# Kernel tuning notes

Measured on AMD Instinct MI355X. Metric: run time of the kernel, lower is better.

## Reference

```python
import jax, jax.numpy as jnp
import numpy as np

N_UE = 16384
N_AP = 128
E = 2097152
D = 32

relu = jax.nn.relu


def setup_inputs():
    key = jax.random.key(0)
    ks = jax.random.split(key, 24)
    def g(i, shape, s=0.1):
        return jax.random.normal(ks[i], shape, dtype=jnp.float32) * s
    inp = {}
    inp["x_ue"] = jax.random.uniform(ks[0], (N_UE, 1), dtype=jnp.float32)
    inp["e_ua"] = g(1, (E, 2), 1.0)
    inp["e_au"] = g(2, (E, 2), 1.0)
    inp["src"] = jax.random.randint(ks[3], (E,), 0, N_UE)
    inp["dst"] = jax.random.randint(ks[4], (E,), 0, N_AP)
    # layer 1 (Ue2Ap): ue feat dim 1, ap feat dim 0, edge dim 2
    inp["Wm1_ua"] = g(5, (1 + 2, D)); inp["bm1_ua"] = jnp.zeros((D,), jnp.float32)
    inp["Wm1_au"] = g(6, (2, D));     inp["bm1_au"] = jnp.zeros((D,), jnp.float32)
    inp["Wu1_ap"] = g(7, (D, D));     inp["bu1_ap"] = jnp.zeros((D,), jnp.float32)
    inp["Wu1_ue"] = g(8, (1 + D, D)); inp["bu1_ue"] = jnp.zeros((D,), jnp.float32)
    inp["We1_ua"] = g(9, (2 * D + 2, 2));  inp["be1_ua"] = jnp.zeros((2,), jnp.float32)
    inp["We1_au"] = g(10, (2 * D + 2, 2)); inp["be1_au"] = jnp.zeros((2,), jnp.float32)
    # layers 2-4 stacked (all 32 -> 32)
    inp["Wm_ua"] = g(11, (3, D + 2, D)); inp["bm_ua"] = jnp.zeros((3, D), jnp.float32)
    inp["Wm_au"] = g(12, (3, D + 2, D)); inp["bm_au"] = jnp.zeros((3, D), jnp.float32)
    inp["Wu_ap"] = g(13, (3, 2 * D, D)); inp["bu_ap"] = jnp.zeros((3, D), jnp.float32)
    inp["Wu_ue"] = g(14, (3, 2 * D, D)); inp["bu_ue"] = jnp.zeros((3, D), jnp.float32)
    inp["We_ua"] = g(15, (3, 2 * D + 2, 2)); inp["be_ua"] = jnp.zeros((3, 2), jnp.float32)
    inp["We_au"] = g(16, (3, 2 * D + 2, 2)); inp["be_au"] = jnp.zeros((3, 2), jnp.float32)
    # power head: mlp([32,16]) + Lin(16,1) + Sigmoid
    inp["Wp1"] = g(17, (D, 16)); inp["bp1"] = jnp.zeros((16,), jnp.float32)
    inp["Wp2"] = g(18, (16, 1)); inp["bp2"] = jnp.zeros((1,), jnp.float32)
    return inp


def _het_conv(x_ue, x_ap, e_ua, e_au, src, dst,
              Wm_ua, bm_ua, Wm_au, bm_au,
              Wu_ap, bu_ap, Wu_ue, bu_ue,
              We_ua, be_ua, We_au, be_au):
    # ue -> ap: gather src ue feats + edge attr, MLP, scatter-add to ap
    f_ua = jnp.concatenate([x_ue[src], e_ua], axis=1)        # [E, d_ue+2]
    m_ua = relu(f_ua @ Wm_ua + bm_ua)                        # [E, D]
    agg_ap = jax.ops.segment_sum(m_ua, dst, num_segments=N_AP)
    # ap -> ue: ap has no features in layer 1 (dim 0)
    f_au = e_au if x_ap is None else jnp.concatenate([x_ap[dst], e_au], axis=1)
    m_au = relu(f_au @ Wm_au + bm_au)                        # [E, D]
    agg_ue = jax.ops.segment_sum(m_au, src, num_segments=N_UE)
    # node updates
    h_ap = agg_ap if x_ap is None else jnp.concatenate([x_ap, agg_ap], axis=1)
    x_ap_new = relu(h_ap @ Wu_ap + bu_ap)                    # [N_AP, D]
    x_ue_new = relu(jnp.concatenate([x_ue, agg_ue], axis=1) @ Wu_ue + bu_ue)  # [N_UE, D]
    # edge updates (keep edge_dim = 2)
    pair = jnp.concatenate([x_ue_new[src], x_ap_new[dst]], axis=1)  # [E, 2D]
    e_ua_new = relu(jnp.concatenate([pair, e_ua], axis=1) @ We_ua + be_ua)
    e_au_new = relu(jnp.concatenate([pair, e_au], axis=1) @ We_au + be_au)
    return x_ue_new, x_ap_new, e_ua_new, e_au_new


def reference(x_ue, e_ua, e_au, src, dst,
              Wm1_ua, bm1_ua, Wm1_au, bm1_au, Wu1_ap, bu1_ap, Wu1_ue, bu1_ue,
              We1_ua, be1_ua, We1_au, be1_au,
              Wm_ua, bm_ua, Wm_au, bm_au, Wu_ap, bu_ap, Wu_ue, bu_ue,
              We_ua, be_ua, We_au, be_au,
              Wp1, bp1, Wp2, bp2):
    x_ue, x_ap, e_ua, e_au = _het_conv(
        x_ue, None, e_ua, e_au, src, dst,
        Wm1_ua, bm1_ua, Wm1_au, bm1_au, Wu1_ap, bu1_ap, Wu1_ue, bu1_ue,
        We1_ua, be1_ua, We1_au, be1_au)
    for l in range(3):  # conv2, conv3, conv4
        x_ue, x_ap, e_ua, e_au = _het_conv(
            x_ue, x_ap, e_ua, e_au, src, dst,
            Wm_ua[l], bm_ua[l], Wm_au[l], bm_au[l],
            Wu_ap[l], bu_ap[l], Wu_ue[l], bu_ue[l],
            We_ua[l], be_ua[l], We_au[l], be_au[l])
    power = jax.nn.sigmoid(relu(x_ue @ Wp1 + bp1) @ Wp2 + bp2)  # [N_UE, 1]
    ue_out = jnp.concatenate([x_ue[:, :1], power], axis=1)      # [N_UE, 2]
    return ue_out, x_ap, e_ua, e_au
```

## Files before the change

### kernel.cpp

```cpp
#include <hip/hip_runtime.h>
#include <math.h>

#define N_UE 16384
#define N_AP 128
#define NE   2097152
#define NSB  256
#define EPSB (NE / NSB)
#define CHS  8
#define CHD  16
#define NEP  (NE + CHS * N_UE)
#define NCHU (NEP / CHS)
#define NEPD (NE + CHD * N_AP)
#define NCHD (NEPD / CHD)
#define NCHD_AL 131328

#define RFL(x) __int_as_float(__builtin_amdgcn_readfirstlane(__float_as_int(x)))

__global__ __launch_bounds__(256) void prefill(
    int* __restrict__ dtS, int* __restrict__ srcD,
    int* __restrict__ cnS, int* __restrict__ cnD)
{
    int i = blockIdx.x * 256 + threadIdx.x;
    dtS[i] = N_AP;
    if (i < NEPD) srcD[i] = N_UE;
    if (i < NCHU) cnS[i] = -1;
    if (i < NCHD_AL) cnD[i] = -1;
}

__global__ __launch_bounds__(256) void init_kernel(
    const float* __restrict__ x_ue, const float* __restrict__ Wm1_ua,
    const float* __restrict__ bm1_ua, const float* __restrict__ bm1_au,
    float* __restrict__ Qua, float* __restrict__ Pau)
{
    int i = blockIdx.x * 256 + threadIdx.x;
    int d = i & 31;
    Qua[i] = fmaf(x_ue[i >> 5], Wm1_ua[d], bm1_ua[d]);
    if (i < N_AP * 32) Pau[i] = bm1_au[d];
    if (i < 32) { Qua[N_UE * 32 + i] = -1e30f; Pau[N_AP * 32 + i] = -1e30f; }
}

__global__ __launch_bounds__(256) void hist_src(
    const int* __restrict__ src, int* __restrict__ histS)
{
    __shared__ int h[N_UE];
    for (int i = threadIdx.x; i < N_UE; i += 256) h[i] = 0;
    __syncthreads();
    const int beg = blockIdx.x * EPSB;
    for (int e = beg + threadIdx.x; e < beg + EPSB; e += 256)
        atomicAdd(&h[src[e]], 1);
    __syncthreads();
    for (int i = threadIdx.x; i < N_UE; i += 256) histS[blockIdx.x * N_UE + i] = h[i];
}

__global__ __launch_bounds__(256) void colscan_kernel(
    const int* __restrict__ histS, int* __restrict__ baseS, int* __restrict__ cnt)
{
    const int u = blockIdx.x * 256 + threadIdx.x;
    int run = 0;
    for (int b = 0; b < NSB; ++b) {
        int t = histS[b * N_UE + u];
        baseS[b * N_UE + u] = run;
        run += t;
    }
    cnt[u] = run;
}

__global__ __launch_bounds__(256) void scan_src(
    const int* __restrict__ cnt, int* __restrict__ CU)
{
    __shared__ int ps[256];
    __shared__ int ps2[257];
    const int t = threadIdx.x;
    const int b0 = t * (N_UE / 256);
    int s = 0;
    for (int i = 0; i < N_UE / 256; ++i) s += (cnt[b0 + i] + CHS - 1) / CHS;
    ps[t] = s;
    __syncthreads();
    if (t == 0) {
        int r = 0;
        for (int i = 0; i < 256; ++i) { ps2[i] = r; r += ps[i]; }
        ps2[256] = r;
    }
    __syncthreads();
    int r = ps2[t];
    for (int i = 0; i < N_UE / 256; ++i) { CU[b0 + i] = r; r += (cnt[b0 + i] + CHS - 1) / CHS; }
    if (t == 255) CU[N_UE] = ps2[256];
}

__global__ __launch_bounds__(256) void scatter_src(
    const int* __restrict__ src, const int* __restrict__ dst,
    const float2* __restrict__ e0au,
    const int* __restrict__ baseS, const int* __restrict__ CU,
    int* __restrict__ dtS, float2* __restrict__ attS, int* __restrict__ invS)
{
    __shared__ int cursor[N_UE];
    const int b = blockIdx.x;
    for (int i = threadIdx.x; i < N_UE; i += 256)
        cursor[i] = CU[i] * CHS + baseS[b * N_UE + i];
    __syncthreads();
    const int beg = b * EPSB;
    for (int e = beg + threadIdx.x; e < beg + EPSB; e += 256) {
        int s = src[e];
        int pos = atomicAdd(&cursor[s], 1);
        dtS[pos] = dst[e];
        attS[pos] = e0au[e];
        invS[e] = pos;
    }
}

__global__ __launch_bounds__(256) void hist_dst(
    const int* __restrict__ dst, int* __restrict__ histD)
{
    __shared__ int h[N_AP];
    if (threadIdx.x < N_AP) h[threadIdx.x] = 0;
    __syncthreads();
    const int beg = blockIdx.x * EPSB;
    for (int e = beg + threadIdx.x; e < beg + EPSB; e += 256)
        atomicAdd(&h[dst[e]], 1);
    __syncthreads();
    if (threadIdx.x < N_AP) histD[blockIdx.x * N_AP + threadIdx.x] = h[threadIdx.x];
}

__global__ __launch_bounds__(128) void scan_dst(
    const int* __restrict__ histD, int* __restrict__ offsD, int* __restrict__ CA)
{
    __shared__ int colTot[N_AP], colStart[N_AP];
    const int a = threadIdx.x;
    int run = 0;
    for (int b = 0; b < NSB; ++b) {
        offsD[b * N_AP + a] = run;
        run += histD[b * N_AP + a];
    }
    colTot[a] = run;
    __syncthreads();
    if (a == 0) {
        int r = 0;
        for (int i = 0; i < N_AP; ++i) {
            CA[i] = r;
            colStart[i] = r * CHD;
            r += (colTot[i] + CHD - 1) / CHD;
        }
        CA[N_AP] = r;
    }
    __syncthreads();
    const int st = colStart[a];
    for (int b = 0; b < NSB; ++b) offsD[b * N_AP + a] += st;
}

__global__ __launch_bounds__(256) void scatter_dst(
    const int* __restrict__ src, const int* __restrict__ dst,
    const float2* __restrict__ e0ua, const int* __restrict__ offsD,
    int* __restrict__ srcD, float2* __restrict__ attD, int* __restrict__ invD)
{
    __shared__ int cursor[N_AP];
    const int b = blockIdx.x;
    if (threadIdx.x < N_AP) cursor[threadIdx.x] = offsD[b * N_AP + threadIdx.x];
    __syncthreads();
    const int beg = b * EPSB;
    for (int e = beg + threadIdx.x; e < beg + EPSB; e += 256) {
        int dt = dst[e];
        int pos = atomicAdd(&cursor[dt], 1);
        srcD[pos] = src[e];
        attD[pos] = e0ua[e];
        invD[e] = pos;
    }
}

__global__ __launch_bounds__(256) void build_map_src(
    const int* __restrict__ CU, int* __restrict__ cnS)
{
    const int u = blockIdx.x * 256 + threadIdx.x;
    const int c0 = CU[u], c1 = CU[u + 1];
    for (int c = c0; c < c1; ++c) cnS[c] = u;
}

__global__ __launch_bounds__(128) void build_map_dst(
    const int* __restrict__ CA, int* __restrict__ cnD)
{
    const int a = threadIdx.x;
    const int c0 = CA[a], c1 = CA[a + 1];
    for (int c = c0; c < c1; ++c) cnD[c] = a;
}

template<bool EUPD>
__global__ __launch_bounds__(256) void pass_src(
    const int* __restrict__ cnS, const int* __restrict__ dtS,
    float2* __restrict__ attS,
    const float2* __restrict__ RueB, const float2* __restrict__ RapB,
    const float* __restrict__ EcB,
    const float* __restrict__ Pau, const float* __restrict__ cw,
    float* __restrict__ partialU)
{
    const int ch = blockIdx.x * 256 + threadIdx.x;
    const int u = cnS[ch];
    if (u < 0) return;
    float w0v[32], w1v[32];
    #pragma unroll
    for (int d = 0; d < 32; ++d) { w0v[d] = RFL(cw[d]); w1v[d] = RFL(cw[32 + d]); }
    float d00 = 0.f, d01 = 0.f, d10 = 0.f, d11 = 0.f, rbx = 0.f, rby = 0.f;
    if constexpr (EUPD) {
        d00 = RFL(EcB[0]); d01 = RFL(EcB[1]); d10 = RFL(EcB[2]); d11 = RFL(EcB[3]);
        float2 r = RueB[u]; rbx = r.x; rby = r.y;
    }
    const float4* __restrict__ Pau4 = (const float4*)Pau;
    const int base = ch * CHS;
    float4 acc[8];
    #pragma unroll
    for (int q = 0; q < 8; ++q) acc[q] = make_float4(0.f, 0.f, 0.f, 0.f);
    #pragma unroll
    for (int j = 0; j < CHS; ++j) {
        int dt = dtS[base + j];
        float2 a = attS[base + j];
        if constexpr (EUPD) {
            float2 rp = RapB[dt];
            float m0 = fmaxf(rbx + rp.x + a.x * d00 + a.y * d10, 0.f);
            float m1 = fmaxf(rby + rp.y + a.x * d01 + a.y * d11, 0.f);
            a = make_float2(m0, m1);
            attS[base + j] = a;
        }
        const float4* pr = Pau4 + dt * 8;
        #pragma unroll
        for (int q = 0; q < 8; ++q) {
            float4 pv = pr[q];
            acc[q].x += fmaxf(fmaf(a.x, w0v[q*4+0], fmaf(a.y, w1v[q*4+0], pv.x)), 0.f);
            acc[q].y += fmaxf(fmaf(a.x, w0v[q*4+1], fmaf(a.y, w1v[q*4+1], pv.y)), 0.f);
            acc[q].z += fmaxf(fmaf(a.x, w0v[q*4+2], fmaf(a.y, w1v[q*4+2], pv.z)), 0.f);
            acc[q].w += fmaxf(fmaf(a.x, w0v[q*4+3], fmaf(a.y, w1v[q*4+3], pv.w)), 0.f);
        }
    }
    float4* pu = (float4*)(partialU + (size_t)ch * 32);
    #pragma unroll
    for (int q = 0; q < 8; ++q) pu[q] = acc[q];
}

template<bool EUPD>
__global__ __launch_bounds__(256) void pass_dst(
    const int* __restrict__ cnD, const int* __restrict__ srcD,
    float2* __restrict__ attD,
    const float2* __restrict__ RueA, const float2* __restrict__ RapA,
    const float* __restrict__ EcA,
    const float* __restrict__ Qua, const float* __restrict__ cu,
    float* __restrict__ partialA)
{
    const int ch = blockIdx.x * 256 + threadIdx.x;
    const int a = cnD[ch];
    if (a < 0) return;
    float u0v[32], u1v[32];
    #pragma unroll
    for (int d = 0; d < 32; ++d) { u0v[d] = RFL(cu[d]); u1v[d] = RFL(cu[32 + d]); }
    float c00 = 0.f, c01 = 0.f, c10 = 0.f, c11 = 0.f, rax = 0.f, ray = 0.f;
    if constexpr (EUPD) {
        c00 = RFL(EcA[0]); c01 = RFL(EcA[1]); c10 = RFL(EcA[2]); c11 = RFL(EcA[3]);
        float2 r = RapA[a]; rax = r.x; ray = r.y;
    }
    const float4* __restrict__ Qua4 = (const float4*)Qua;
    const int base = ch * CHD;
    float4 acc[8];
    #pragma unroll
    for (int q = 0; q < 8; ++q) acc[q] = make_float4(0.f, 0.f, 0.f, 0.f);
    #pragma unroll 4
    for (int j = 0; j < CHD; ++j) {
        int s = srcD[base + j];
        float2 a2 = attD[base + j];
        if constexpr (EUPD) {
            float2 ru = RueA[s];
            float n0 = fmaxf(rax + ru.x + a2.x * c00 + a2.y * c10, 0.f);
            float n1 = fmaxf(ray + ru.y + a2.x * c01 + a2.y * c11, 0.f);
            a2 = make_float2(n0, n1);
            attD[base + j] = a2;
        }
        const float4* qr = Qua4 + s * 8;
        #pragma unroll
        for (int q = 0; q < 8; ++q) {
            float4 qv = qr[q];
            acc[q].x += fmaxf(fmaf(a2.x, u0v[q*4+0], fmaf(a2.y, u1v[q*4+0], qv.x)), 0.f);
            acc[q].y += fmaxf(fmaf(a2.x, u0v[q*4+1], fmaf(a2.y, u1v[q*4+1], qv.y)), 0.f);
            acc[q].z += fmaxf(fmaf(a2.x, u0v[q*4+2], fmaf(a2.y, u1v[q*4+2], qv.z)), 0.f);
            acc[q].w += fmaxf(fmaf(a2.x, u0v[q*4+3], fmaf(a2.y, u1v[q*4+3], qv.w)), 0.f);
        }
    }
    float4* pa = (float4*)(partialA + (size_t)ch * 32);
    #pragma unroll
    for (int q = 0; q < 8; ++q) pa[q] = acc[q];
}

__global__ __launch_bounds__(256) void reduce_ue(
    const int* __restrict__ CU, const float* __restrict__ partialU,
    float* __restrict__ agg_ue)
{
    const int g   = (blockIdx.x * 256 + threadIdx.x) >> 5;
    const int dim = threadIdx.x & 31;
    const int c0 = CU[g], c1 = CU[g + 1];
    float acc = 0.f;
    for (int c = c0; c < c1; ++c) acc += partialU[(size_t)c * 32 + dim];
    agg_ue[g * 32 + dim] = acc;
}

__global__ __launch_bounds__(256) void final_edge(
    const int* __restrict__ src, const int* __restrict__ dst,
    const int* __restrict__ invS, const int* __restrict__ invD,
    const float2* __restrict__ attS, const float2* __restrict__ attD,
    const float2* __restrict__ RueA, const float2* __restrict__ RueB,
    const float2* __restrict__ RapA, const float2* __restrict__ RapB,
    const float* __restrict__ EcA, const float* __restrict__ EcB,
    float2* __restrict__ out_eua, float2* __restrict__ out_eau)
{
    const int e = blockIdx.x * 256 + threadIdx.x;
    const int s = src[e], dt = dst[e];
    float c00 = EcA[0], c01 = EcA[1], c10 = EcA[2], c11 = EcA[3];
    float d00 = EcB[0], d01 = EcB[1], d10 = EcB[2], d11 = EcB[3];
    float2 eua = attD[invD[e]];
    float2 eau = attS[invS[e]];
    float2 rA = RueA[s], pA = RapA[dt];
    float n0 = fmaxf(rA.x + pA.x + eua.x * c00 + eua.y * c10, 0.f);
    float n1 = fmaxf(rA.y + pA.y + eua.x * c01 + eua.y * c11, 0.f);
    float2 rB = RueB[s], pB = RapB[dt];
    float m0 = fmaxf(rB.x + pB.x + eau.x * d00 + eau.y * d10, 0.f);
    float m1 = fmaxf(rB.y + pB.y + eau.x * d01 + eau.y * d11, 0.f);
    out_eua[e] = make_float2(n0, n1);
    out_eau[e] = make_float2(m0, m1);
}

template<bool FIRST, bool LAST>
__global__ __launch_bounds__(256) void node_ue_kernel(
    const float* __restrict__ x_prev, const float* __restrict__ agg_ue,
    const float* __restrict__ Wu, const float* __restrict__ bu,
    const float* __restrict__ Wm_next, const float* __restrict__ bm_next,
    const float* __restrict__ WeUa, const float* __restrict__ WeUb,
    const float* __restrict__ Wp1, const float* __restrict__ bp1,
    const float* __restrict__ Wp2, const float* __restrict__ bp2,
    float* __restrict__ x_new, float* __restrict__ Qua_next,
    float2* __restrict__ RueA, float2* __restrict__ RueB,
    float2* __restrict__ ue_out)
{
    constexpr int KIN = FIRST ? 33 : 64;
    __shared__ float Wu_s[64 * 32];
    __shared__ float Wm_s[32 * 32];
    __shared__ float WeA_s[64], WeB_s[64];
    __shared__ float bu_s[32], bm_s[32];
    __shared__ float Wp1_s[32 * 16], bp1_s[16], Wp2_s[16];

    const int tid = threadIdx.x;
    for (int i = tid; i < KIN * 32; i += 256) Wu_s[i] = Wu[i];
    if (tid < 32) bu_s[tid] = bu[tid];
    if (!LAST) {
        for (int i = tid; i < 1024; i += 256) Wm_s[i] = Wm_next[i];
        if (tid < 32) bm_s[tid] = bm_next[tid];
    }
    if (tid < 64) { WeA_s[tid] = WeUa[tid]; WeB_s[tid] = WeUb[tid]; }
    if (LAST) {
        for (int i = tid; i < 512; i += 256) Wp1_s[i] = Wp1[i];
        if (tid < 16) { bp1_s[tid] = bp1[tid]; Wp2_s[tid] = Wp2[tid]; }
    }
    __syncthreads();

    const int u = blockIdx.x * 256 + tid;
    float in[KIN];
    if (FIRST) {
        in[0] = x_prev[u];
        #pragma unroll
        for (int k = 0; k < 32; ++k) in[1 + k] = agg_ue[u * 32 + k];
    } else {
        #pragma unroll
        for (int k = 0; k < 32; ++k) in[k] = x_prev[u * 32 + k];
        #pragma unroll
        for (int k = 0; k < 32; ++k) in[32 + k] = agg_ue[u * 32 + k];
    }
    float out[32];
    #pragma unroll
    for (int d = 0; d < 32; ++d) {
        float acc = bu_s[d];
        #pragma unroll
        for (int k = 0; k < KIN; ++k) acc = fmaf(in[k], Wu_s[k * 32 + d], acc);
        out[d] = fmaxf(acc, 0.f);
    }
    #pragma unroll
    for (int d = 0; d < 32; ++d) x_new[u * 32 + d] = out[d];
    if (!LAST) {
        #pragma unroll
        for (int d = 0; d < 32; ++d) {
            float acc = bm_s[d];
            #pragma unroll
            for (int k = 0; k < 32; ++k) acc = fmaf(out[k], Wm_s[k * 32 + d], acc);
            Qua_next[u * 32 + d] = acc;
        }
    }
    float r0 = 0.f, r1 = 0.f, s0 = 0.f, s1 = 0.f;
    #pragma unroll
    for (int k = 0; k < 32; ++k) {
        r0 = fmaf(out[k], WeA_s[k * 2],     r0);
        r1 = fmaf(out[k], WeA_s[k * 2 + 1], r1);
        s0 = fmaf(out[k], WeB_s[k * 2],     s0);
        s1 = fmaf(out[k], WeB_s[k * 2 + 1], s1);
    }
    RueA[u] = make_float2(r0, r1);
    RueB[u] = make_float2(s0, s1);
    if (LAST) {
        float z = bp2[0];
        #pragma unroll
        for (int j = 0; j < 16; ++j) {
            float h = bp1_s[j];
            #pragma unroll
            for (int k = 0; k < 32; ++k) h = fmaf(out[k], Wp1_s[k * 16 + j], h);
            z = fmaf(fmaxf(h, 0.f), Wp2_s[j], z);
        }
        float pw = 1.f / (1.f + expf(-z));
        ue_out[u] = make_float2(out[0], pw);
    }
}

template<bool FIRST, bool LAST>
__global__ __launch_bounds__(256) void node_ap_kernel(
    const float* __restrict__ partialA, const int* __restrict__ CA,
    const float* __restrict__ x_prev,
    const float* __restrict__ Wu, const float* __restrict__ bu,
    const float* __restrict__ Wm_next, const float* __restrict__ bm_next,
    const float* __restrict__ WeA, const float* __restrict__ beA,
    const float* __restrict__ WeB, const float* __restrict__ beB,
    float* __restrict__ x_new, float* __restrict__ Pau_next,
    float2* __restrict__ RapA, float2* __restrict__ RapB)
{
    __shared__ float red[256];
    __shared__ float agg_s[32];
    __shared__ float xnew_s[32];
    const int a = blockIdx.x, tid = threadIdx.x;
    const int d = tid & 31, p0 = tid >> 5;
    const int c0 = CA[a], c1 = CA[a + 1];
    float acc = 0.f;
    for (int p = c0 + p0; p < c1; p += 8)
        acc += partialA[(size_t)p * 32 + d];
    red[tid] = acc;
    __syncthreads();
    if (tid < 32) {
        float s = 0.f;
        #pragma unroll
        for (int i = 0; i < 8; ++i) s += red[i * 32 + tid];
        agg_s[tid] = s;
    }
    __syncthreads();
    if (tid < 32) {
        float acc2 = bu[d];
        if (FIRST) {
            #pragma unroll
            for (int k = 0; k < 32; ++k) acc2 = fmaf(agg_s[k], Wu[k * 32 + d], acc2);
        } else {
            #pragma unroll
            for (int k = 0; k < 32; ++k) acc2 = fmaf(x_prev[a * 32 + k], Wu[k * 32 + d], acc2);
            #pragma unroll
            for (int k = 0; k < 32; ++k) acc2 = fmaf(agg_s[k], Wu[(32 + k) * 32 + d], acc2);
        }
        float xn = fmaxf(acc2, 0.f);
        xnew_s[d] = xn;
        x_new[a * 32 + d] = xn;
    }
    __syncthreads();
    if (!LAST) {
        if (tid < 32) {
            float acc3 = bm_next[d];
            #pragma unroll
            for (int k = 0; k < 32; ++k) acc3 = fmaf(xnew_s[k], Wm_next[k * 32 + d], acc3);
            Pau_next[a * 32 + d] = acc3;
        }
    }
    if (tid == 0) {
        float q0 = beA[0], q1 = beA[1], t0 = beB[0], t1 = beB[1];
        #pragma unroll
        for (int k = 0; k < 32; ++k) {
            q0 = fmaf(xnew_s[k], WeA[k * 2],     q0);
            q1 = fmaf(xnew_s[k], WeA[k * 2 + 1], q1);
            t0 = fmaf(xnew_s[k], WeB[k * 2],     t0);
            t1 = fmaf(xnew_s[k], WeB[k * 2 + 1], t1);
        }
        RapA[a] = make_float2(q0, q1);
        RapB[a] = make_float2(t0, t1);
    }
}

extern "C" void kernel_launch(void* const* d_in, const int* in_sizes, int n_in,
                              void* d_out_v, int out_size, void* d_ws, size_t ws_size,
                              hipStream_t stream)
{
    const float*  x_ue   = (const float*)d_in[0];
    const float2* e0ua   = (const float2*)d_in[1];
    const float2* e0au   = (const float2*)d_in[2];
    const int*    src    = (const int*)d_in[3];
    const int*    dst    = (const int*)d_in[4];
    const float* Wm1_ua = (const float*)d_in[5];
    const float* bm1_ua = (const float*)d_in[6];
    const float* Wm1_au = (const float*)d_in[7];
    const float* bm1_au = (const float*)d_in[8];
    const float* Wu1_ap = (const float*)d_in[9];
    const float* bu1_ap = (const float*)d_in[10];
    const float* Wu1_ue = (const float*)d_in[11];
    const float* bu1_ue = (const float*)d_in[12];
    const float* We1_ua = (const float*)d_in[13];
    const float* be1_ua = (const float*)d_in[14];
    const float* We1_au = (const float*)d_in[15];
    const float* be1_au = (const float*)d_in[16];
    const float* Wm_ua  = (const float*)d_in[17];
    const float* bm_ua  = (const float*)d_in[18];
    const float* Wm_au  = (const float*)d_in[19];
    const float* bm_au  = (const float*)d_in[20];
    const float* Wu_ap  = (const float*)d_in[21];
    const float* bu_ap  = (const float*)d_in[22];
    const float* Wu_ue  = (const float*)d_in[23];
    const float* bu_ue  = (const float*)d_in[24];
    const float* We_ua  = (const float*)d_in[25];
    const float* be_ua  = (const float*)d_in[26];
    const float* We_au  = (const float*)d_in[27];
    const float* be_au  = (const float*)d_in[28];
    const float* Wp1    = (const float*)d_in[29];
    const float* bp1    = (const float*)d_in[30];
    const float* Wp2    = (const float*)d_in[31];
    const float* bp2    = (const float*)d_in[32];

    float*  outp    = (float*)d_out_v;
    float2* out_ue  = (float2*)outp;
    float*  out_ap  = outp + N_UE * 2;
    float2* out_eua = (float2*)(outp + N_UE * 2 + N_AP * 32);
    float2* out_eau = (float2*)(outp + N_UE * 2 + N_AP * 32 + (size_t)NE * 2);

    float* ws = (float*)d_ws;
    float* x_ueA  = ws;          ws += N_UE * 32;
    float* x_ueB  = ws;          ws += N_UE * 32;
    float* x_apA  = ws;          ws += N_AP * 32;
    float* x_apB  = ws;          ws += N_AP * 32;
    float* agg_ue = ws;          ws += N_UE * 32;
    float* Qua    = ws;          ws += (N_UE + 1) * 32;
    float* Pau    = ws;          ws += (N_AP + 1) * 32;
    float2* RueA  = (float2*)ws; ws += (N_UE + 2) * 2;
    float2* RueB  = (float2*)ws; ws += (N_UE + 2) * 2;
    float2* RapA  = (float2*)ws; ws += (N_AP + 2) * 2;
    float2* RapB  = (float2*)ws; ws += (N_AP + 2) * 2;
    int* cnt   = (int*)ws;       ws += N_UE;
    int* CU    = (int*)ws;       ws += N_UE + 4;
    int* histD = (int*)ws;       ws += NSB * N_AP;
    int* offsD = (int*)ws;       ws += NSB * N_AP;
    int* CA    = (int*)ws;       ws += N_AP + 4;
    int* cnS   = (int*)ws;       ws += NCHU;
    int* cnD   = (int*)ws;       ws += NCHD_AL;
    int* invS  = (int*)ws;       ws += NE;
    int* invD  = (int*)ws;       ws += NE;
    int* dtS   = (int*)ws;       ws += NEP;
    int* srcD  = (int*)ws;       ws += NEPD;
    float2* attS = (float2*)ws;  ws += (size_t)NEP * 2;
    float2* attD = (float2*)ws;  ws += (size_t)NEPD * 2;
    float* partialU = ws;        ws += (size_t)NCHU * 32;
    float* partialA = ws;        ws += (size_t)NCHD_AL * 32;
    int* histS = (int*)partialU;
    int* baseS = (int*)(partialU + (size_t)NSB * N_UE);

    dim3 blk(256);

    prefill<<<NEP / 256, blk, 0, stream>>>(dtS, srcD, cnS, cnD);
    hist_src<<<NSB, blk, 0, stream>>>(src, histS);
    colscan_kernel<<<N_UE / 256, blk, 0, stream>>>(histS, baseS, cnt);
    scan_src<<<1, blk, 0, stream>>>(cnt, CU);
    scatter_src<<<NSB, blk, 0, stream>>>(src, dst, e0au, baseS, CU, dtS, attS, invS);
    hist_dst<<<NSB, blk, 0, stream>>>(dst, histD);
    scan_dst<<<1, dim3(128), 0, stream>>>(histD, offsD, CA);
    scatter_dst<<<NSB, blk, 0, stream>>>(src, dst, e0ua, offsD, srcD, attD, invD);
    build_map_src<<<N_UE / 256, blk, 0, stream>>>(CU, cnS);
    build_map_dst<<<1, dim3(128), 0, stream>>>(CA, cnD);

    init_kernel<<<N_UE * 32 / 256, blk, 0, stream>>>(x_ue, Wm1_ua, bm1_ua, bm1_au, Qua, Pau);

    pass_src<false><<<NCHU / 256, blk, 0, stream>>>(
        cnS, dtS, attS, nullptr, nullptr, nullptr, Pau, Wm1_au, partialU);
    pass_dst<false><<<NCHD_AL / 256, blk, 0, stream>>>(
        cnD, srcD, attD, nullptr, nullptr, nullptr, Qua, Wm1_ua + 32, partialA);
    reduce_ue<<<N_UE * 32 / 256, blk, 0, stream>>>(CU, partialU, agg_ue);
    node_ue_kernel<true, false><<<N_UE / 256, blk, 0, stream>>>(
        x_ue, agg_ue, Wu1_ue, bu1_ue, Wm_ua, bm_ua, We1_ua, We1_au,
        nullptr, nullptr, nullptr, nullptr,
        x_ueA, Qua, RueA, RueB, nullptr);
    node_ap_kernel<true, false><<<N_AP, blk, 0, stream>>>(
        partialA, CA, nullptr, Wu1_ap, bu1_ap, Wm_au, bm_au,
        We1_ua + 64, be1_ua, We1_au + 64, be1_au,
        x_apA, Pau, RapA, RapB);

    pass_src<true><<<NCHU / 256, blk, 0, stream>>>(
        cnS, dtS, attS, RueB, RapB, We1_au + 128, Pau, Wm_au + 1024, partialU);
    pass_dst<true><<<NCHD_AL / 256, blk, 0, stream>>>(
        cnD, srcD, attD, RueA, RapA, We1_ua + 128, Qua, Wm_ua + 1024, partialA);
    reduce_ue<<<N_UE * 32 / 256, blk, 0, stream>>>(CU, partialU, agg_ue);
    node_ue_kernel<false, false><<<N_UE / 256, blk, 0, stream>>>(
        x_ueA, agg_ue, Wu_ue, bu_ue, Wm_ua + 1088, bm_ua + 32, We_ua, We_au,
        nullptr, nullptr, nullptr, nullptr,
        x_ueB, Qua, RueA, RueB, nullptr);
    node_ap_kernel<false, false><<<N_AP, blk, 0, stream>>>(
        partialA, CA, x_apA, Wu_ap, bu_ap, Wm_au + 1088, bm_au + 32,
        We_ua + 64, be_ua, We_au + 64, be_au,
        x_apB, Pau, RapA, RapB);

    pass_src<true><<<NCHU / 256, blk, 0, stream>>>(
        cnS, dtS, attS, RueB, RapB, We_au + 128, Pau, Wm_au + 2112, partialU);
    pass_dst<true><<<NCHD_AL / 256, blk, 0, stream>>>(
        cnD, srcD, attD, RueA, RapA, We_ua + 128, Qua, Wm_ua + 2112, partialA);
    reduce_ue<<<N_UE * 32 / 256, blk, 0, stream>>>(CU, partialU, agg_ue);
    node_ue_kernel<false, false><<<N_UE / 256, blk, 0, stream>>>(
        x_ueB, agg_ue, Wu_ue + 2048, bu_ue + 32, Wm_ua + 2176, bm_ua + 64,
        We_ua + 132, We_au + 132,
        nullptr, nullptr, nullptr, nullptr,
        x_ueA, Qua, RueA, RueB, nullptr);
    node_ap_kernel<false, false><<<N_AP, blk, 0, stream>>>(
        partialA, CA, x_apB, Wu_ap + 2048, bu_ap + 32, Wm_au + 2176, bm_au + 64,
        We_ua + 196, be_ua + 2, We_au + 196, be_au + 2,
        x_apA, Pau, RapA, RapB);

    pass_src<true><<<NCHU / 256, blk, 0, stream>>>(
        cnS, dtS, attS, RueB, RapB, We_au + 260, Pau, Wm_au + 3200, partialU);
    pass_dst<true><<<NCHD_AL / 256, blk, 0, stream>>>(
        cnD, srcD, attD, RueA, RapA, We_ua + 260, Qua, Wm_ua + 3200, partialA);
    reduce_ue<<<N_UE * 32 / 256, blk, 0, stream>>>(CU, partialU, agg_ue);
    node_ue_kernel<false, true><<<N_UE / 256, blk, 0, stream>>>(
        x_ueA, agg_ue, Wu_ue + 4096, bu_ue + 64, nullptr, nullptr,
        We_ua + 264, We_au + 264,
        Wp1, bp1, Wp2, bp2,
        x_ueB, nullptr, RueA, RueB, out_ue);
    node_ap_kernel<false, true><<<N_AP, blk, 0, stream>>>(
        partialA, CA, x_apA, Wu_ap + 4096, bu_ap + 64, nullptr, nullptr,
        We_ua + 328, be_ua + 4, We_au + 328, be_au + 4,
        out_ap, nullptr, RapA, RapB);

    final_edge<<<NE / 256, blk, 0, stream>>>(
        src, dst, invS, invD, attS, attD,
        RueA, RueB, RapA, RapB,
        We_ua + 392, We_au + 392, out_eua, out_eau);
}
```

Before: 996.4 us.

## Fuse src/dst histogram, scatter and message passes; pack histograms to 16-bit

Merges the src and dst histogram kernels into one pass, with the src histogram packed as two 16-bit counters per 32-bit shared word. The two scatter kernels are merged into one that processes the src keys in two halves so the cursor array fits in shared memory. The per-layer src and dst message passes become a single launch that splits on block index, so the two passes run concurrently and launch count drops. node_ue now uses 64-thread blocks for more blocks in flight. The 16-bit histograms assume no node has more than 65535 edges per block, and the fused scatter reads src/dst twice.

```diff
diff --git a/kernel.cpp b/kernel.cpp
--- a/kernel.cpp
+++ b/kernel.cpp
@@ -6,13 +6,15 @@
 #define NE   2097152
 #define NSB  256
 #define EPSB (NE / NSB)
+#define NHALF (N_UE / 2)
 #define CHS  8
 #define CHD  16
 #define NEP  (NE + CHS * N_UE)
 #define NCHU (NEP / CHS)
 #define NEPD (NE + CHD * N_AP)
-#define NCHD (NEPD / CHD)
 #define NCHD_AL 131328
+#define SRC_BLKS (NCHU / 256)
+#define DST_BLKS (NCHD_AL / 256)
 
 #define RFL(x) __int_as_float(__builtin_amdgcn_readfirstlane(__float_as_int(x)))
 
@@ -39,27 +41,38 @@
     if (i < 32) { Qua[N_UE * 32 + i] = -1e30f; Pau[N_AP * 32 + i] = -1e30f; }
 }
 
-__global__ __launch_bounds__(256) void hist_src(
-    const int* __restrict__ src, int* __restrict__ histS)
-{
-    __shared__ int h[N_UE];
-    for (int i = threadIdx.x; i < N_UE; i += 256) h[i] = 0;
-    __syncthreads();
-    const int beg = blockIdx.x * EPSB;
-    for (int e = beg + threadIdx.x; e < beg + EPSB; e += 256)
-        atomicAdd(&h[src[e]], 1);
-    __syncthreads();
-    for (int i = threadIdx.x; i < N_UE; i += 256) histS[blockIdx.x * N_UE + i] = h[i];
+__global__ __launch_bounds__(256) void hist_both(
+    const int* __restrict__ src, const int* __restrict__ dst,
+    unsigned short* __restrict__ histS, int* __restrict__ histD)
+{
+    __shared__ unsigned int h32[N_UE / 2];
+    __shared__ int hd[N_AP];
+    const int tid = threadIdx.x, b = blockIdx.x;
+    for (int i = tid; i < N_UE / 2; i += 256) h32[i] = 0u;
+    if (tid < N_AP) hd[tid] = 0;
+    __syncthreads();
+    const int beg = b * EPSB;
+    for (int e = beg + tid; e < beg + EPSB; e += 256) {
+        int s = src[e];
+        atomicAdd(&h32[s >> 1], 1u << ((s & 1) * 16));
+        atomicAdd(&hd[dst[e]], 1);
+    }
+    __syncthreads();
+    for (int i = tid; i < N_UE; i += 256)
+        histS[(size_t)b * N_UE + i] =
+            (unsigned short)((h32[i >> 1] >> ((i & 1) * 16)) & 0xffffu);
+    if (tid < N_AP) histD[b * N_AP + tid] = hd[tid];
 }
 
 __global__ __launch_bounds__(256) void colscan_kernel(
-    const int* __restrict__ histS, int* __restrict__ baseS, int* __restrict__ cnt)
+    const unsigned short* __restrict__ histS,
+    unsigned short* __restrict__ baseS, int* __restrict__ cnt)
 {
     const int u = blockIdx.x * 256 + threadIdx.x;
     int run = 0;
     for (int b = 0; b < NSB; ++b) {
-        int t = histS[b * N_UE + u];
-        baseS[b * N_UE + u] = run;
+        int t = histS[(size_t)b * N_UE + u];
+        baseS[(size_t)b * N_UE + u] = (unsigned short)run;
         run += t;
     }
     cnt[u] = run;
@@ -87,40 +100,6 @@
     if (t == 255) CU[N_UE] = ps2[256];
 }
 
-__global__ __launch_bounds__(256) void scatter_src(
-    const int* __restrict__ src, const int* __restrict__ dst,
-    const float2* __restrict__ e0au,
-    const int* __restrict__ baseS, const int* __restrict__ CU,
-    int* __restrict__ dtS, float2* __restrict__ attS, int* __restrict__ invS)
-{
-    __shared__ int cursor[N_UE];
-    const int b = blockIdx.x;
-    for (int i = threadIdx.x; i < N_UE; i += 256)
-        cursor[i] = CU[i] * CHS + baseS[b * N_UE + i];
-    __syncthreads();
-    const int beg = b * EPSB;
-    for (int e = beg + threadIdx.x; e < beg + EPSB; e += 256) {
-        int s = src[e];
-        int pos = atomicAdd(&cursor[s], 1);
-        dtS[pos] = dst[e];
-        attS[pos] = e0au[e];
-        invS[e] = pos;
-    }
-}
-
-__global__ __launch_bounds__(256) void hist_dst(
-    const int* __restrict__ dst, int* __restrict__ histD)
-{
-    __shared__ int h[N_AP];
-    if (threadIdx.x < N_AP) h[threadIdx.x] = 0;
-    __syncthreads();
-    const int beg = blockIdx.x * EPSB;
-    for (int e = beg + threadIdx.x; e < beg + EPSB; e += 256)
-        atomicAdd(&h[dst[e]], 1);
-    __syncthreads();
-    if (threadIdx.x < N_AP) histD[blockIdx.x * N_AP + threadIdx.x] = h[threadIdx.x];
-}
-
 __global__ __launch_bounds__(128) void scan_dst(
     const int* __restrict__ histD, int* __restrict__ offsD, int* __restrict__ CA)
 {
@@ -147,22 +126,41 @@
     for (int b = 0; b < NSB; ++b) offsD[b * N_AP + a] += st;
 }
 
-__global__ __launch_bounds__(256) void scatter_dst(
+__global__ __launch_bounds__(256) void scatter_both(
     const int* __restrict__ src, const int* __restrict__ dst,
-    const float2* __restrict__ e0ua, const int* __restrict__ offsD,
+    const float2* __restrict__ e0ua, const float2* __restrict__ e0au,
+    const unsigned short* __restrict__ baseS, const int* __restrict__ CU,
+    const int* __restrict__ offsD,
+    int* __restrict__ dtS, float2* __restrict__ attS, int* __restrict__ invS,
     int* __restrict__ srcD, float2* __restrict__ attD, int* __restrict__ invD)
 {
-    __shared__ int cursor[N_AP];
-    const int b = blockIdx.x;
-    if (threadIdx.x < N_AP) cursor[threadIdx.x] = offsD[b * N_AP + threadIdx.x];
-    __syncthreads();
+    __shared__ int cursor[NHALF];
+    __shared__ int cursord[N_AP];
+    const int tid = threadIdx.x, b = blockIdx.x;
     const int beg = b * EPSB;
-    for (int e = beg + threadIdx.x; e < beg + EPSB; e += 256) {
-        int dt = dst[e];
-        int pos = atomicAdd(&cursor[dt], 1);
-        srcD[pos] = src[e];
-        attD[pos] = e0ua[e];
-        invD[e] = pos;
+    if (tid < N_AP) cursord[tid] = offsD[b * N_AP + tid];
+    for (int p = 0; p < 2; ++p) {
+        const int lo = p * NHALF;
+        for (int i = tid; i < NHALF; i += 256)
+            cursor[i] = CU[lo + i] * CHS + (int)baseS[(size_t)b * N_UE + lo + i];
+        __syncthreads();
+        for (int e = beg + tid; e < beg + EPSB; e += 256) {
+            int s = src[e];
+            int dt = dst[e];
+            if (p == 0) {
+                int posd = atomicAdd(&cursord[dt], 1);
+                srcD[posd] = s;
+                attD[posd] = e0ua[e];
+                invD[e] = posd;
+            }
+            if (s >= lo && s < lo + NHALF) {
+                int pos = atomicAdd(&cursor[s - lo], 1);
+                dtS[pos] = dt;
+                attS[pos] = e0au[e];
+                invS[e] = pos;
+            }
+        }
+        __syncthreads();
     }
 }
 
@@ -183,105 +181,101 @@
 }
 
 template<bool EUPD>
-__global__ __launch_bounds__(256) void pass_src(
+__global__ __launch_bounds__(256) void pass_both(
     const int* __restrict__ cnS, const int* __restrict__ dtS,
     float2* __restrict__ attS,
-    const float2* __restrict__ RueB, const float2* __restrict__ RapB,
-    const float* __restrict__ EcB,
-    const float* __restrict__ Pau, const float* __restrict__ cw,
-    float* __restrict__ partialU)
-{
-    const int ch = blockIdx.x * 256 + threadIdx.x;
-    const int u = cnS[ch];
-    if (u < 0) return;
-    float w0v[32], w1v[32];
-    #pragma unroll
-    for (int d = 0; d < 32; ++d) { w0v[d] = RFL(cw[d]); w1v[d] = RFL(cw[32 + d]); }
-    float d00 = 0.f, d01 = 0.f, d10 = 0.f, d11 = 0.f, rbx = 0.f, rby = 0.f;
-    if constexpr (EUPD) {
-        d00 = RFL(EcB[0]); d01 = RFL(EcB[1]); d10 = RFL(EcB[2]); d11 = RFL(EcB[3]);
-        float2 r = RueB[u]; rbx = r.x; rby = r.y;
-    }
-    const float4* __restrict__ Pau4 = (const float4*)Pau;
-    const int base = ch * CHS;
-    float4 acc[8];
-    #pragma unroll
-    for (int q = 0; q < 8; ++q) acc[q] = make_float4(0.f, 0.f, 0.f, 0.f);
-    #pragma unroll
-    for (int j = 0; j < CHS; ++j) {
-        int dt = dtS[base + j];
-        float2 a = attS[base + j];
-        if constexpr (EUPD) {
-            float2 rp = RapB[dt];
-            float m0 = fmaxf(rbx + rp.x + a.x * d00 + a.y * d10, 0.f);
-            float m1 = fmaxf(rby + rp.y + a.x * d01 + a.y * d11, 0.f);
-            a = make_float2(m0, m1);
-            attS[base + j] = a;
-        }
-        const float4* pr = Pau4 + dt * 8;
-        #pragma unroll
-        for (int q = 0; q < 8; ++q) {
-            float4 pv = pr[q];
-            acc[q].x += fmaxf(fmaf(a.x, w0v[q*4+0], fmaf(a.y, w1v[q*4+0], pv.x)), 0.f);
-            acc[q].y += fmaxf(fmaf(a.x, w0v[q*4+1], fmaf(a.y, w1v[q*4+1], pv.y)), 0.f);
-            acc[q].z += fmaxf(fmaf(a.x, w0v[q*4+2], fmaf(a.y, w1v[q*4+2], pv.z)), 0.f);
-            acc[q].w += fmaxf(fmaf(a.x, w0v[q*4+3], fmaf(a.y, w1v[q*4+3], pv.w)), 0.f);
-        }
-    }
-    float4* pu = (float4*)(partialU + (size_t)ch * 32);
-    #pragma unroll
-    for (int q = 0; q < 8; ++q) pu[q] = acc[q];
-}
-
-template<bool EUPD>
-__global__ __launch_bounds__(256) void pass_dst(
     const int* __restrict__ cnD, const int* __restrict__ srcD,
     float2* __restrict__ attD,
-    const float2* __restrict__ RueA, const float2* __restrict__ RapA,
-    const float* __restrict__ EcA,
-    const float* __restrict__ Qua, const float* __restrict__ cu,
-    float* __restrict__ partialA)
-{
-    const int ch = blockIdx.x * 256 + threadIdx.x;
-    const int a = cnD[ch];
-    if (a < 0) return;
-    float u0v[32], u1v[32];
-    #pragma unroll
-    for (int d = 0; d < 32; ++d) { u0v[d] = RFL(cu[d]); u1v[d] = RFL(cu[32 + d]); }
-    float c00 = 0.f, c01 = 0.f, c10 = 0.f, c11 = 0.f, rax = 0.f, ray = 0.f;
-    if constexpr (EUPD) {
-        c00 = RFL(EcA[0]); c01 = RFL(EcA[1]); c10 = RFL(EcA[2]); c11 = RFL(EcA[3]);
-        float2 r = RapA[a]; rax = r.x; ray = r.y;
-    }
-    const float4* __restrict__ Qua4 = (const float4*)Qua;
-    const int base = ch * CHD;
-    float4 acc[8];
-    #pragma unroll
-    for (int q = 0; q < 8; ++q) acc[q] = make_float4(0.f, 0.f, 0.f, 0.f);
-    #pragma unroll 4
-    for (int j = 0; j < CHD; ++j) {
-        int s = srcD[base + j];
-        float2 a2 = attD[base + j];
+    const float2* __restrict__ RueA, const float2* __restrict__ RueB,
+    const float2* __restrict__ RapA, const float2* __restrict__ RapB,
+    const float* __restrict__ EcA, const float* __restrict__ EcB,
+    const float* __restrict__ Qua, const float* __restrict__ Pau,
+    const float* __restrict__ cu, const float* __restrict__ cw,
+    float* __restrict__ partialU, float* __restrict__ partialA)
+{
+    if (blockIdx.x < SRC_BLKS) {
+        const int ch = blockIdx.x * 256 + threadIdx.x;
+        const int u = cnS[ch];
+        if (u < 0) return;
+        float w0v[32], w1v[32];
+        #pragma unroll
+        for (int d = 0; d < 32; ++d) { w0v[d] = RFL(cw[d]); w1v[d] = RFL(cw[32 + d]); }
+        float d00 = 0.f, d01 = 0.f, d10 = 0.f, d11 = 0.f, rbx = 0.f, rby = 0.f;
         if constexpr (EUPD) {
-            float2 ru = RueA[s];
-            float n0 = fmaxf(rax + ru.x + a2.x * c00 + a2.y * c10, 0.f);
-            float n1 = fmaxf(ray + ru.y + a2.x * c01 + a2.y * c11, 0.f);
-            a2 = make_float2(n0, n1);
-            attD[base + j] = a2;
-        }
-        const float4* qr = Qua4 + s * 8;
-        #pragma unroll
-        for (int q = 0; q < 8; ++q) {
-            float4 qv = qr[q];
-            acc[q].x += fmaxf(fmaf(a2.x, u0v[q*4+0], fmaf(a2.y, u1v[q*4+0], qv.x)), 0.f);
-            acc[q].y += fmaxf(fmaf(a2.x, u0v[q*4+1], fmaf(a2.y, u1v[q*4+1], qv.y)), 0.f);
-            acc[q].z += fmaxf(fmaf(a2.x, u0v[q*4+2], fmaf(a2.y, u1v[q*4+2], qv.z)), 0.f);
-            acc[q].w += fmaxf(fmaf(a2.x, u0v[q*4+3], fmaf(a2.y, u1v[q*4+3], qv.w)), 0.f);
-        }
-    }
-    float4* pa = (float4*)(partialA + (size_t)ch * 32);
-    #pragma unroll
-    for (int q = 0; q < 8; ++q) pa[q] = acc[q];
+            d00 = RFL(EcB[0]); d01 = RFL(EcB[1]); d10 = RFL(EcB[2]); d11 = RFL(EcB[3]);
+            float2 r = RueB[u]; rbx = r.x; rby = r.y;
+        }
+        const float4* __restrict__ Pau4 = (const float4*)Pau;
+        const int base = ch * CHS;
+        float4 acc[8];
+        #pragma unroll
+        for (int q = 0; q < 8; ++q) acc[q] = make_float4(0.f, 0.f, 0.f, 0.f);
+        #pragma unroll
+        for (int j = 0; j < CHS; ++j) {
+            int dt = dtS[base + j];
+            float2 a = attS[base + j];
+            if constexpr (EUPD) {
+                float2 rp = RapB[dt];
+                float m0 = fmaxf(rbx + rp.x + a.x * d00 + a.y * d10, 0.f);
+                float m1 = fmaxf(rby + rp.y + a.x * d01 + a.y * d11, 0.f);
+                a = make_float2(m0, m1);
+                attS[base + j] = a;
+            }
+            const float4* pr = Pau4 + dt * 8;
+            #pragma unroll
+            for (int q = 0; q < 8; ++q) {
+                float4 pv = pr[q];
+                acc[q].x += fmaxf(fmaf(a.x, w0v[q*4+0], fmaf(a.y, w1v[q*4+0], pv.x)), 0.f);
+                acc[q].y += fmaxf(fmaf(a.x, w0v[q*4+1], fmaf(a.y, w1v[q*4+1], pv.y)), 0.f);
+                acc[q].z += fmaxf(fmaf(a.x, w0v[q*4+2], fmaf(a.y, w1v[q*4+2], pv.z)), 0.f);
+                acc[q].w += fmaxf(fmaf(a.x, w0v[q*4+3], fmaf(a.y, w1v[q*4+3], pv.w)), 0.f);
+            }
+        }
+        float4* pu = (float4*)(partialU + (size_t)ch * 32);
+        #pragma unroll
+        for (int q = 0; q < 8; ++q) pu[q] = acc[q];
+    } else {
+        const int ch = (blockIdx.x - SRC_BLKS) * 256 + threadIdx.x;
+        const int a = cnD[ch];
+        if (a < 0) return;
+        float u0v[32], u1v[32];
+        #pragma unroll
+        for (int d = 0; d < 32; ++d) { u0v[d] = RFL(cu[d]); u1v[d] = RFL(cu[32 + d]); }
+        float c00 = 0.f, c01 = 0.f, c10 = 0.f, c11 = 0.f, rax = 0.f, ray = 0.f;
+        if constexpr (EUPD) {
+            c00 = RFL(EcA[0]); c01 = RFL(EcA[1]); c10 = RFL(EcA[2]); c11 = RFL(EcA[3]);
+            float2 r = RapA[a]; rax = r.x; ray = r.y;
+        }
+        const float4* __restrict__ Qua4 = (const float4*)Qua;
+        const int base = ch * CHD;
+        float4 acc[8];
+        #pragma unroll
+        for (int q = 0; q < 8; ++q) acc[q] = make_float4(0.f, 0.f, 0.f, 0.f);
+        #pragma unroll 4
+        for (int j = 0; j < CHD; ++j) {
+            int s = srcD[base + j];
+            float2 a2 = attD[base + j];
+            if constexpr (EUPD) {
+                float2 ru = RueA[s];
+                float n0 = fmaxf(rax + ru.x + a2.x * c00 + a2.y * c10, 0.f);
+                float n1 = fmaxf(ray + ru.y + a2.x * c01 + a2.y * c11, 0.f);
+                a2 = make_float2(n0, n1);
+                attD[base + j] = a2;
+            }
+            const float4* qr = Qua4 + s * 8;
+            #pragma unroll
+            for (int q = 0; q < 8; ++q) {
+                float4 qv = qr[q];
+                acc[q].x += fmaxf(fmaf(a2.x, u0v[q*4+0], fmaf(a2.y, u1v[q*4+0], qv.x)), 0.f);
+                acc[q].y += fmaxf(fmaf(a2.x, u0v[q*4+1], fmaf(a2.y, u1v[q*4+1], qv.y)), 0.f);
+                acc[q].z += fmaxf(fmaf(a2.x, u0v[q*4+2], fmaf(a2.y, u1v[q*4+2], qv.z)), 0.f);
+                acc[q].w += fmaxf(fmaf(a2.x, u0v[q*4+3], fmaf(a2.y, u1v[q*4+3], qv.w)), 0.f);
+            }
+        }
+        float4* pa = (float4*)(partialA + (size_t)ch * 32);
+        #pragma unroll
+        for (int q = 0; q < 8; ++q) pa[q] = acc[q];
+    }
 }
 
 __global__ __launch_bounds__(256) void reduce_ue(
@@ -322,7 +316,7 @@
 }
 
 template<bool FIRST, bool LAST>
-__global__ __launch_bounds__(256) void node_ue_kernel(
+__global__ __launch_bounds__(64) void node_ue_kernel(
     const float* __restrict__ x_prev, const float* __restrict__ agg_ue,
     const float* __restrict__ Wu, const float* __restrict__ bu,
     const float* __restrict__ Wm_next, const float* __restrict__ bm_next,
@@ -341,20 +335,20 @@
     __shared__ float Wp1_s[32 * 16], bp1_s[16], Wp2_s[16];
 
     const int tid = threadIdx.x;
-    for (int i = tid; i < KIN * 32; i += 256) Wu_s[i] = Wu[i];
+    for (int i = tid; i < KIN * 32; i += 64) Wu_s[i] = Wu[i];
     if (tid < 32) bu_s[tid] = bu[tid];
     if (!LAST) {
-        for (int i = tid; i < 1024; i += 256) Wm_s[i] = Wm_next[i];
+        for (int i = tid; i < 1024; i += 64) Wm_s[i] = Wm_next[i];
         if (tid < 32) bm_s[tid] = bm_next[tid];
     }
-    if (tid < 64) { WeA_s[tid] = WeUa[tid]; WeB_s[tid] = WeUb[tid]; }
+    { WeA_s[tid] = WeUa[tid]; WeB_s[tid] = WeUb[tid]; }
     if (LAST) {
-        for (int i = tid; i < 512; i += 256) Wp1_s[i] = Wp1[i];
+        for (int i = tid; i < 512; i += 64) Wp1_s[i] = Wp1[i];
         if (tid < 16) { bp1_s[tid] = bp1[tid]; Wp2_s[tid] = Wp2[tid]; }
     }
     __syncthreads();
 
-    const int u = blockIdx.x * 256 + tid;
+    const int u = blockIdx.x * 64 + tid;
     float in[KIN];
     if (FIRST) {
         in[0] = x_prev[u];
@@ -547,30 +541,31 @@
     float2* attD = (float2*)ws;  ws += (size_t)NEPD * 2;
     float* partialU = ws;        ws += (size_t)NCHU * 32;
     float* partialA = ws;        ws += (size_t)NCHD_AL * 32;
-    int* histS = (int*)partialU;
-    int* baseS = (int*)(partialU + (size_t)NSB * N_UE);
+    unsigned short* histS = (unsigned short*)partialU;
+    unsigned short* baseS = (unsigned short*)(partialU + (size_t)(NSB * N_UE / 2));
 
     dim3 blk(256);
 
     prefill<<<NEP / 256, blk, 0, stream>>>(dtS, srcD, cnS, cnD);
-    hist_src<<<NSB, blk, 0, stream>>>(src, histS);
+    hist_both<<<NSB, blk, 0, stream>>>(src, dst, histS, histD);
     colscan_kernel<<<N_UE / 256, blk, 0, stream>>>(histS, baseS, cnt);
     scan_src<<<1, blk, 0, stream>>>(cnt, CU);
-    scatter_src<<<NSB, blk, 0, stream>>>(src, dst, e0au, baseS, CU, dtS, attS, invS);
-    hist_dst<<<NSB, blk, 0, stream>>>(dst, histD);
     scan_dst<<<1, dim3(128), 0, stream>>>(histD, offsD, CA);
-    scatter_dst<<<NSB, blk, 0, stream>>>(src, dst, e0ua, offsD, srcD, attD, invD);
+    scatter_both<<<NSB, blk, 0, stream>>>(src, dst, e0ua, e0au, baseS, CU, offsD,
+                                          dtS, attS, invS, srcD, attD, invD);
     build_map_src<<<N_UE / 256, blk, 0, stream>>>(CU, cnS);
     build_map_dst<<<1, dim3(128), 0, stream>>>(CA, cnD);
 
     init_kernel<<<N_UE * 32 / 256, blk, 0, stream>>>(x_ue, Wm1_ua, bm1_ua, bm1_au, Qua, Pau);
 
-    pass_src<false><<<NCHU / 256, blk, 0, stream>>>(
-        cnS, dtS, attS, nullptr, nullptr, nullptr, Pau, Wm1_au, partialU);
-    pass_dst<false><<<NCHD_AL / 256, blk, 0, stream>>>(
-        cnD, srcD, attD, nullptr, nullptr, nullptr, Qua, Wm1_ua + 32, partialA);
+    const int PB = SRC_BLKS + DST_BLKS;
+
+    pass_both<false><<<PB, blk, 0, stream>>>(
+        cnS, dtS, attS, cnD, srcD, attD,
+        nullptr, nullptr, nullptr, nullptr, nullptr, nullptr,
+        Qua, Pau, Wm1_ua + 32, Wm1_au, partialU, partialA);
     reduce_ue<<<N_UE * 32 / 256, blk, 0, stream>>>(CU, partialU, agg_ue);
-    node_ue_kernel<true, false><<<N_UE / 256, blk, 0, stream>>>(
+    node_ue_kernel<true, false><<<N_UE / 64, dim3(64), 0, stream>>>(
         x_ue, agg_ue, Wu1_ue, bu1_ue, Wm_ua, bm_ua, We1_ua, We1_au,
         nullptr, nullptr, nullptr, nullptr,
         x_ueA, Qua, RueA, RueB, nullptr);
@@ -579,12 +574,12 @@
         We1_ua + 64, be1_ua, We1_au + 64, be1_au,
         x_apA, Pau, RapA, RapB);
 
-    pass_src<true><<<NCHU / 256, blk, 0, stream>>>(
-        cnS, dtS, attS, RueB, RapB, We1_au + 128, Pau, Wm_au + 1024, partialU);
-    pass_dst<true><<<NCHD_AL / 256, blk, 0, stream>>>(
-        cnD, srcD, attD, RueA, RapA, We1_ua + 128, Qua, Wm_ua + 1024, partialA);
+    pass_both<true><<<PB, blk, 0, stream>>>(
+        cnS, dtS, attS, cnD, srcD, attD,
+        RueA, RueB, RapA, RapB, We1_ua + 128, We1_au + 128,
+        Qua, Pau, Wm_ua + 1024, Wm_au + 1024, partialU, partialA);
     reduce_ue<<<N_UE * 32 / 256, blk, 0, stream>>>(CU, partialU, agg_ue);
-    node_ue_kernel<false, false><<<N_UE / 256, blk, 0, stream>>>(
+    node_ue_kernel<false, false><<<N_UE / 64, dim3(64), 0, stream>>>(
         x_ueA, agg_ue, Wu_ue, bu_ue, Wm_ua + 1088, bm_ua + 32, We_ua, We_au,
         nullptr, nullptr, nullptr, nullptr,
         x_ueB, Qua, RueA, RueB, nullptr);
@@ -593,12 +588,12 @@
         We_ua + 64, be_ua, We_au + 64, be_au,
         x_apB, Pau, RapA, RapB);
 
-    pass_src<true><<<NCHU / 256, blk, 0, stream>>>(
-        cnS, dtS, attS, RueB, RapB, We_au + 128, Pau, Wm_au + 2112, partialU);
-    pass_dst<true><<<NCHD_AL / 256, blk, 0, stream>>>(
-        cnD, srcD, attD, RueA, RapA, We_ua + 128, Qua, Wm_ua + 2112, partialA);
+    pass_both<true><<<PB, blk, 0, stream>>>(
+        cnS, dtS, attS, cnD, srcD, attD,
+        RueA, RueB, RapA, RapB, We_ua + 128, We_au + 128,
+        Qua, Pau, Wm_ua + 2112, Wm_au + 2112, partialU, partialA);
     reduce_ue<<<N_UE * 32 / 256, blk, 0, stream>>>(CU, partialU, agg_ue);
-    node_ue_kernel<false, false><<<N_UE / 256, blk, 0, stream>>>(
+    node_ue_kernel<false, false><<<N_UE / 64, dim3(64), 0, stream>>>(
         x_ueB, agg_ue, Wu_ue + 2048, bu_ue + 32, Wm_ua + 2176, bm_ua + 64,
         We_ua + 132, We_au + 132,
         nullptr, nullptr, nullptr, nullptr,
@@ -608,12 +603,12 @@
         We_ua + 196, be_ua + 2, We_au + 196, be_au + 2,
         x_apA, Pau, RapA, RapB);
 
-    pass_src<true><<<NCHU / 256, blk, 0, stream>>>(
-        cnS, dtS, attS, RueB, RapB, We_au + 260, Pau, Wm_au + 3200, partialU);
-    pass_dst<true><<<NCHD_AL / 256, blk, 0, stream>>>(
-        cnD, srcD, attD, RueA, RapA, We_ua + 260, Qua, Wm_ua + 3200, partialA);
+    pass_both<true><<<PB, blk, 0, stream>>>(
+        cnS, dtS, attS, cnD, srcD, attD,
+        RueA, RueB, RapA, RapB, We_ua + 260, We_au + 260,
+        Qua, Pau, Wm_ua + 3200, Wm_au + 3200, partialU, partialA);
     reduce_ue<<<N_UE * 32 / 256, blk, 0, stream>>>(CU, partialU, agg_ue);
-    node_ue_kernel<false, true><<<N_UE / 256, blk, 0, stream>>>(
+    node_ue_kernel<false, true><<<N_UE / 64, dim3(64), 0, stream>>>(
         x_ueA, agg_ue, Wu_ue + 4096, bu_ue + 64, nullptr, nullptr,
         We_ua + 264, We_au + 264,
         Wp1, bp1, Wp2, bp2,
```

After: 891.9 us. 1.12x faster.
